# Kernel optimization log

Hardware: AMD Instinct MI355X
Metric: run time of the kernel (lower is better)

Reference implementation:

```python
import jax, jax.numpy as jnp
import numpy as np

C = 256          # channels
KS = 7           # kernel_size
G = 256          # groups (defaults to channels)
HID = C // 4     # hidden = channels // reduction
BN_EPS = 1e-5


def setup_inputs() -> dict:
    key = jax.random.key(0)
    ks = jax.random.split(key, 4)
    B, H, W = 4, 64, 64
    return {
        "x": jax.random.normal(ks[0], (B, C, H, W), jnp.float32),
        "reduce_w": jax.random.normal(ks[1], (HID, C), jnp.float32) / np.float32(np.sqrt(C)),
        "bn_gamma": jnp.ones((HID,), jnp.float32),
        "bn_beta": jnp.zeros((HID,), jnp.float32),
        "bn_mean": jnp.zeros((HID,), jnp.float32),
        "bn_var": jnp.ones((HID,), jnp.float32),
        "kproj_w": jax.random.normal(ks[2], (KS * KS * G, HID), jnp.float32) / np.float32(np.sqrt(HID)),
        "kproj_b": jnp.zeros((KS * KS * G,), jnp.float32),
    }


def _kernels(x, reduce_w, bn_gamma, bn_beta, bn_mean, bn_var, kproj_w, kproj_b):
    # 1x1 conv -> BN (eval mode) -> ReLU -> 1x1 conv, then per-pixel L2 kernel norm
    B, _, H, W = x.shape
    h = jnp.einsum('bchw,oc->bohw', x, reduce_w)
    inv = bn_gamma / jnp.sqrt(bn_var + BN_EPS)
    h = h * inv[None, :, None, None] + (bn_beta - bn_mean * inv)[None, :, None, None]
    h = jax.nn.relu(h)
    ker = jnp.einsum('bchw,oc->bohw', h, kproj_w) + kproj_b[None, :, None, None]
    ker = ker.reshape(B, G, KS * KS, H, W)           # (B, G, k*k, H, W)
    # kernel_norm == 'l2': zero-mean + unit L2 norm over the k*k taps
    ker = ker - ker.mean(axis=2, keepdims=True)
    denom = jnp.maximum(jnp.sqrt(jnp.sum(ker * ker, axis=2, keepdims=True)), 1e-6)
    return ker / denom


def reference(x, reduce_w, bn_gamma, bn_beta, bn_mean, bn_var, kproj_w, kproj_b):
    # get_kernels is under @torch.no_grad() in the original -> stop_gradient
    ker = jax.lax.stop_gradient(
        _kernels(x, reduce_w, bn_gamma, bn_beta, bn_mean, bn_var, kproj_w, kproj_b))
    B, Cc, H, W = x.shape
    pad = KS // 2
    gc = Cc // G  # = 1 for depthwise involution
    xp = jnp.pad(x, ((0, 0), (0, 0), (pad, pad), (pad, pad)))
    xg = xp.reshape(B, G, gc, H + 2 * pad, W + 2 * pad)
    # fused unfold-multiply-accumulate over the k*k taps (no (B,C,k,k,H,W) tensor)
    out = jnp.zeros((B, G, gc, H, W), x.dtype)
    for t in range(KS * KS):
        i, j = divmod(t, KS)
        out = out + xg[:, :, :, i:i + H, j:j + W] * ker[:, :, t][:, :, None]
    return out.reshape(B, Cc, H, W)
```

## Files before the change

### kernel.cpp

```cpp
#include <hip/hip_runtime.h>


#define C_    256
#define HID_  64
#define KS_   7
#define KK_   49
#define G_    256
#define H_    64
#define W_    64
#define HW_   4096
#define BN_EPS 1e-5f

typedef __attribute__((ext_vector_type(8)))  short bf16x8;
typedef __attribute__((ext_vector_type(4)))  float f32x4;
typedef __attribute__((ext_vector_type(16))) float f32x16;
typedef __attribute__((ext_vector_type(2)))  unsigned uv2;

__device__ __forceinline__ ushort f2bf(float f) {
    unsigned u = __float_as_uint(f);
    return (ushort)((u + 0x7fffu + ((u >> 16) & 1u)) >> 16);
}
__device__ __forceinline__ float bf2f(ushort s) {
    return __uint_as_float((unsigned)s << 16);
}
__device__ __forceinline__ float xor32p(float v) {
#if __has_builtin(__builtin_amdgcn_permlane32_swap)
    uv2 r = __builtin_amdgcn_permlane32_swap(__float_as_uint(v), __float_as_uint(v),
                                             false, false);
    return (__uint_as_float(r[0]) + __uint_as_float(r[1])) - v;
#else
    return __shfl_xor(v, 32);
#endif
}

__global__ __launch_bounds__(256) void prep_kernel(
    const float* __restrict__ kw, const float* __restrict__ kb,
    const float* __restrict__ reduce_w,
    const float* __restrict__ bn_gamma, const float* __restrict__ bn_beta,
    const float* __restrict__ bn_mean, const float* __restrict__ bn_var,
    ushort* __restrict__ kwb, float* __restrict__ rwT, float* __restrict__ betp,
    float* __restrict__ kbp)
{
    const int bid = blockIdx.x;
    if (bid < 256) {
        int idx  = bid * 256 + threadIdx.x;
        int base = idx * 16;
        int g    = base >> 12;
        int rem  = base & 4095;
        int t    = rem >> 6;
        int k0   = rem & 63;
        if (t >= 49 && ((t - 49) & 3) <= 1) return;
        union { ushort s[16]; uint4 v[2]; } u;
        if (t < KK_) {
            const float* src = kw + ((size_t)(g * KK_ + t)) * HID_ + k0;
            #pragma unroll
            for (int i = 0; i < 16; ++i) u.s[i] = f2bf(src[i]);
        } else {
            #pragma unroll
            for (int i = 0; i < 16; ++i) u.s[i] = 0;
        }
        uint4* dst = (uint4*)(kwb + base);
        dst[0] = u.v[0];
        dst[1] = u.v[1];
    } else if (bid == 256) {
        int k = threadIdx.x;
        #pragma unroll 1
        for (int o = 0; o < HID_; ++o) {
            float inv = bn_gamma[o] * rsqrtf(bn_var[o] + BN_EPS);
            rwT[k * HID_ + o] = reduce_w[o * C_ + k] * inv;
        }
        if (k < HID_) {
            float inv = bn_gamma[k] * rsqrtf(bn_var[k] + BN_EPS);
            betp[k] = bn_beta[k] - bn_mean[k] * inv;
        }
    } else if (bid == 257) {
        for (int i = threadIdx.x; i < G_ * 64; i += 256) {
            int g = i >> 6, t = i & 63;
            if (t >= 49 && ((t - 49) & 3) == 0) continue;
            kbp[i] = (t < KK_) ? kb[g * KK_ + t] : 0.f;
        }
    } else {
        const int g = bid - 258;
        __shared__ float part[4][64];
        const int k  = threadIdx.x & 63;
        const int pr = threadIdx.x >> 6;
        const int t0 = pr * 13;
        const int t1 = (t0 + 13 < KK_) ? t0 + 13 : KK_;
        float s = 0.f;
        for (int t = t0; t < t1; ++t)
            s += kw[((size_t)(g * KK_ + t)) * HID_ + k];
        part[pr][k] = s;
        __syncthreads();
        if (threadIdx.x < 64) {
            float u = part[0][k] + part[1][k] + part[2][k] + part[3][k];
            ushort uh = f2bf(u);
            ushort ul = f2bf(u - bf2f(uh));
            #pragma unroll
            for (int rr = 0; rr < 4; ++rr) {
                kwb[(size_t)g * 4096 + (49 + rr * 4) * 64 + k] = uh;
                kwb[(size_t)g * 4096 + (50 + rr * 4) * 64 + k] = ul;
            }
            float bs = (k < KK_) ? kb[g * KK_ + k] : 0.f;
            #pragma unroll
            for (int off = 32; off >= 1; off >>= 1) bs += __shfl_xor(bs, off);
            if (k == 0) {
                #pragma unroll
                for (int rr = 0; rr < 4; ++rr) kbp[g * 64 + 49 + rr * 4] = bs;
            }
        }
    }
}

__global__ __launch_bounds__(256) void hv1_kernel(
    const float* __restrict__ x, const float* __restrict__ rwT,
    float* __restrict__ hvp, int npx)
{
    const int lane = threadIdx.x & 63;
    const int wq   = __builtin_amdgcn_readfirstlane(threadIdx.x >> 6);
    const int kq   = blockIdx.y;
    const int p    = blockIdx.x * 64 + lane;
    const int b    = p >> 12;
    const int hw   = p & 4095;

    float acc[16];
    #pragma unroll
    for (int j = 0; j < 16; ++j) acc[j] = 0.f;

    const float* xp = x + ((size_t)b * C_ + kq * 64) * HW_ + hw;
    const float* rw = rwT + (kq * 64) * HID_ + wq * 16;
    #pragma unroll 8
    for (int kk = 0; kk < 64; ++kk) {
        float xk = xp[(size_t)kk * HW_];
        #pragma unroll
        for (int j = 0; j < 16; ++j) acc[j] = fmaf(xk, rw[kk * HID_ + j], acc[j]);
    }
    float* dst = hvp + ((size_t)(kq * 64 + wq * 16)) * npx + p;
    #pragma unroll
    for (int j = 0; j < 16; ++j) dst[(size_t)j * npx] = acc[j];
}

__global__ __launch_bounds__(256) void hv2_kernel(
    const float* __restrict__ hvp, const float* __restrict__ betp,
    ushort* __restrict__ hv, int npx)
{
    const int p  = blockIdx.x * 256 + threadIdx.x;
    const int o0 = blockIdx.y * 4;
    ushort s[4];
    #pragma unroll
    for (int j = 0; j < 4; ++j) {
        float v = 0.f;
        #pragma unroll
        for (int kq = 0; kq < 4; ++kq)
            v += hvp[(size_t)(kq * 64 + o0 + j) * npx + p];
        s[j] = f2bf(fmaxf(v + betp[o0 + j], 0.f));
    }
    uint2 w;
    w.x = (uint)s[0] | ((uint)s[1] << 16);
    w.y = (uint)s[2] | ((uint)s[3] << 16);
    *(uint2*)(hv + (size_t)p * HID_ + o0) = w;
}

__global__ __launch_bounds__(256) void invol_main(
    const float* __restrict__ x, const ushort* __restrict__ hv,
    const ushort* __restrict__ kwb, const float* __restrict__ kbp,
    float* __restrict__ out)
{
    __shared__ float x_s[38][72];
    __shared__ float hs_s[38][64];

    const int tid  = threadIdx.x;
    const int lane = tid & 63;
    const int wave = __builtin_amdgcn_readfirstlane(tid >> 6);
    const int bg   = blockIdx.x;
    const int b    = bg >> 8;
    const int g    = bg & 255;
    const int y0   = blockIdx.y << 5;
    const int l31  = lane & 31;
    const int h4   = (lane >> 5) * 4;
    const int kl16 = (lane >> 5) * 16;

    const float* xg = x + (size_t)bg * HW_;
    for (int idx = tid; idx < 38 * 72; idx += 256) {
        int r = idx / 72, c = idx - r * 72;
        int yy = y0 - 3 + r;
        int cc = c - 3;
        bool v = ((unsigned)yy < 64u) && ((unsigned)cc < 64u);
        x_s[r][c] = v ? xg[yy * 64 + cc] : 0.f;
    }

    bf16x8 ka[2][4];
    const char* kwg = (const char*)kwb + (size_t)g * 8192;
    #pragma unroll
    for (int m = 0; m < 2; ++m)
        #pragma unroll
        for (int s = 0; s < 4; ++s)
            ka[m][s] = *(const bf16x8*)(kwg + (m * 32 + l31) * 128 + s * 32 + kl16);
    f32x4 kv[2][4];
    #pragma unroll
    for (int m = 0; m < 2; ++m)
        #pragma unroll
        for (int q = 0; q < 4; ++q)
            kv[m][q] = *(const f32x4*)(kbp + g * 64 + m * 32 + q * 8 + h4);

    int po0[16], po1[9];
    #pragma unroll
    for (int r = 0; r < 16; ++r) {
        int T = (r & 3) + 8 * (r >> 2) + h4;
        int i = (T * 147) >> 10;
        int j = T - i * 7;
        po0[r] = i * 72 + j + l31;
    }
    #pragma unroll
    for (int r = 0; r < 9; ++r) {
        int T = 32 + (r & 3) + 8 * (r >> 2) + h4;
        int i = (T * 147) >> 10;
        int j = T - i * 7;
        po1[r] = i * 72 + j + l31;
    }

    __syncthreads();

    if (tid < 152) {
        int r  = tid >> 2;
        int c0 = (tid & 3) << 4;
        float v[22];
        #pragma unroll
        for (int i = 0; i < 22; ++i) v[i] = x_s[r][c0 + i];
        float s = v[0] + v[1] + v[2] + v[3] + v[4] + v[5] + v[6];
        hs_s[r][c0] = s;
        #pragma unroll
        for (int c = 1; c < 16; ++c) {
            s += v[c + 6] - v[c - 1];
            hs_s[r][c0 + c] = s;
        }
    }
    __syncthreads();

    const int rowpix0 = (b << 12) + (y0 << 6);

    #pragma unroll 2
    for (int rr = 0; rr < 8; ++rr) {
        const int ry = rr * 4 + wave;

        bf16x8 hb0[4], hb1[4];
        const char* hvrow = (const char*)hv + (size_t)(rowpix0 + (ry << 6)) * 128;
        #pragma unroll
        for (int s = 0; s < 4; ++s) {
            hb0[s] = *(const bf16x8*)(hvrow + l31 * 128 + s * 32 + kl16);
            hb1[s] = *(const bf16x8*)(hvrow + (32 + l31) * 128 + s * 32 + kl16);
        }

        float x2 = hs_s[ry][lane] + hs_s[ry + 1][lane] + hs_s[ry + 2][lane]
                 + hs_s[ry + 3][lane] + hs_s[ry + 4][lane]
                 + hs_s[ry + 5][lane] + hs_s[ry + 6][lane];

        f32x16 acc00, acc01, acc10, acc11;
        #pragma unroll
        for (int q = 0; q < 4; ++q)
            #pragma unroll
            for (int e = 0; e < 4; ++e) {
                acc00[q * 4 + e] = kv[0][q][e];
                acc01[q * 4 + e] = kv[0][q][e];
                acc10[q * 4 + e] = kv[1][q][e];
                acc11[q * 4 + e] = kv[1][q][e];
            }
        #pragma unroll
        for (int s = 0; s < 4; ++s) {
            acc00 = __builtin_amdgcn_mfma_f32_32x32x16_bf16(ka[0][s], hb0[s], acc00, 0, 0, 0);
            acc01 = __builtin_amdgcn_mfma_f32_32x32x16_bf16(ka[0][s], hb1[s], acc01, 0, 0, 0);
            acc10 = __builtin_amdgcn_mfma_f32_32x32x16_bf16(ka[1][s], hb0[s], acc10, 0, 0, 0);
            acc11 = __builtin_amdgcn_mfma_f32_32x32x16_bf16(ka[1][s], hb1[s], acc11, 0, 0, 0);
        }

        float ssq0 = 0.f, ssq1 = 0.f;
        #pragma unroll
        for (int r = 0; r < 16; ++r) {
            ssq0 = fmaf(acc00[r], acc00[r], ssq0);
            ssq1 = fmaf(acc01[r], acc01[r], ssq1);
        }
        #pragma unroll
        for (int r = 0; r < 9; ++r) {
            ssq0 = fmaf(acc10[r], acc10[r], ssq0);
            ssq1 = fmaf(acc11[r], acc11[r], ssq1);
        }
        float mn0 = (acc10[9] + acc10[10]) * (1.f / 49.f);
        float mn1 = (acc11[9] + acc11[10]) * (1.f / 49.f);

        float kx0 = 0.f, kx1 = 0.f;
        const float* xb = &x_s[0][0] + ry * 72;
        #pragma unroll
        for (int r = 0; r < 16; ++r) {
            float xv0 = xb[po0[r]];
            float xv1 = xb[po0[r] + 32];
            kx0 = fmaf(acc00[r], xv0, kx0);
            kx1 = fmaf(acc01[r], xv1, kx1);
        }
        #pragma unroll
        for (int r = 0; r < 9; ++r) {
            float xv0 = xb[po1[r]];
            float xv1 = xb[po1[r] + 32];
            kx0 = fmaf(acc10[r], xv0, kx0);
            kx1 = fmaf(acc11[r], xv1, kx1);
        }

        const bool lo = lane < 32;
        float kx_own = lo ? kx0 : kx1, kx_cr = lo ? kx1 : kx0;
        float ss_own = lo ? ssq0 : ssq1, ss_cr = lo ? ssq1 : ssq0;
        float mo     = lo ? mn0 : mn1;
        float kxo = kx_own + xor32p(kx_cr);
        float sso = ss_own + xor32p(ss_cr);

        float ss = fmaxf(sso - 49.f * mo * mo, 0.f);
        float is = 1.f / fmaxf(sqrtf(ss), 1e-6f);
        out[(size_t)bg * HW_ + ((y0 + ry) << 6) + lane] = (kxo - mo * x2) * is;
    }
}

__global__ __launch_bounds__(256) void hv_kernel(
    const float* __restrict__ x, const float* __restrict__ rwT,
    const float* __restrict__ betp, ushort* __restrict__ hv)
{
    const int lane = threadIdx.x & 63;
    const int q    = __builtin_amdgcn_readfirstlane(threadIdx.x >> 6);
    const int p    = blockIdx.x * 64 + lane;
    const int b    = p >> 12;
    const int hw   = p & 4095;
    float acc[16];
    #pragma unroll
    for (int j = 0; j < 16; ++j) acc[j] = betp[q * 16 + j];
    const float* xp = x + (size_t)b * C_ * HW_ + hw;
    #pragma unroll 8
    for (int k = 0; k < C_; ++k) {
        float xk = xp[(size_t)k * HW_];
        const float* rw = rwT + k * HID_ + q * 16;
        #pragma unroll
        for (int j = 0; j < 16; ++j) acc[j] = fmaf(xk, rw[j], acc[j]);
    }
    union { ushort s[16]; uint4 v[2]; } u;
    #pragma unroll
    for (int j = 0; j < 16; ++j) u.s[j] = f2bf(fmaxf(acc[j], 0.f));
    uint4* dst = (uint4*)(hv + (size_t)p * HID_ + q * 16);
    dst[0] = u.v[0];
    dst[1] = u.v[1];
}

__global__ __launch_bounds__(256) void invol_fallback(
    const float* __restrict__ x, const float* __restrict__ reduce_w,
    const float* __restrict__ bn_gamma, const float* __restrict__ bn_beta,
    const float* __restrict__ bn_mean, const float* __restrict__ bn_var,
    const float* __restrict__ kw, const float* __restrict__ kb,
    float* __restrict__ out)
{
    __shared__ float rwT[C_][HID_ + 4];
    __shared__ float bns[HID_];
    __shared__ float bnb[HID_];
    const int tid = threadIdx.x;
    const int b  = blockIdx.z;
    const int g0 = blockIdx.y * 32;
    const int p  = blockIdx.x * 256 + tid;
    const int py = p >> 6;
    const int px = p & 63;
    #pragma unroll 1
    for (int o = 0; o < HID_; ++o) rwT[tid][o] = reduce_w[o * C_ + tid];
    if (tid < HID_) {
        float inv = bn_gamma[tid] * rsqrtf(bn_var[tid] + BN_EPS);
        bns[tid] = inv;
        bnb[tid] = bn_beta[tid] - bn_mean[tid] * inv;
    }
    __syncthreads();
    float hvv[HID_];
    #pragma unroll
    for (int o = 0; o < HID_; ++o) hvv[o] = 0.f;
    const float* xb = x + (size_t)b * C_ * HW_ + p;
    #pragma unroll 4
    for (int k = 0; k < C_; ++k) {
        float xk = xb[(size_t)k * HW_];
        const float4* wr = (const float4*)&rwT[k][0];
        #pragma unroll
        for (int o4 = 0; o4 < HID_ / 4; ++o4) {
            float4 w = wr[o4];
            hvv[o4*4+0] = fmaf(xk, w.x, hvv[o4*4+0]);
            hvv[o4*4+1] = fmaf(xk, w.y, hvv[o4*4+1]);
            hvv[o4*4+2] = fmaf(xk, w.z, hvv[o4*4+2]);
            hvv[o4*4+3] = fmaf(xk, w.w, hvv[o4*4+3]);
        }
    }
    #pragma unroll
    for (int o = 0; o < HID_; ++o) hvv[o] = fmaxf(fmaf(hvv[o], bns[o], bnb[o]), 0.f);
    #pragma unroll 1
    for (int gi = 0; gi < 32; ++gi) {
        const int g = g0 + gi;
        const float* kwg = kw + (size_t)g * KK_ * HID_;
        float acc[KK_];
        #pragma unroll
        for (int t = 0; t < KK_; ++t) {
            float a = kb[g * KK_ + t];
            const float4* row = (const float4*)(kwg + t * HID_);
            #pragma unroll
            for (int k4 = 0; k4 < HID_ / 4; ++k4) {
                float4 w = row[k4];
                a = fmaf(w.x, hvv[k4*4+0], a);
                a = fmaf(w.y, hvv[k4*4+1], a);
                a = fmaf(w.z, hvv[k4*4+2], a);
                a = fmaf(w.w, hvv[k4*4+3], a);
            }
            acc[t] = a;
        }
        float mean = 0.f;
        #pragma unroll
        for (int t = 0; t < KK_; ++t) mean += acc[t];
        mean *= (1.f / 49.f);
        float ss = 0.f;
        #pragma unroll
        for (int t = 0; t < KK_; ++t) { acc[t] -= mean; ss = fmaf(acc[t], acc[t], ss); }
        float inv = 1.f / fmaxf(sqrtf(ss), 1e-6f);
        const float* xg = x + ((size_t)(b * G_ + g)) * HW_;
        float oacc = 0.f;
        #pragma unroll
        for (int i = 0; i < KS_; ++i) {
            int yv = py + i - 3;
            bool rok = ((unsigned)yv < (unsigned)H_);
            const float* xrow = xg + yv * W_;
            #pragma unroll
            for (int j = 0; j < KS_; ++j) {
                int xx = px + j - 3;
                bool ok = rok && ((unsigned)xx < (unsigned)W_);
                float v = ok ? xrow[xx] : 0.f;
                oacc = fmaf(v, acc[i*7+j], oacc);
            }
        }
        out[((size_t)(b * G_ + g)) * HW_ + p] = oacc * inv;
    }
}

extern "C" void kernel_launch(void* const* d_in, const int* in_sizes, int n_in,
                              void* d_out, int out_size, void* d_ws, size_t ws_size,
                              hipStream_t stream) {
    const float* x        = (const float*)d_in[0];
    const float* reduce_w = (const float*)d_in[1];
    const float* bn_gamma = (const float*)d_in[2];
    const float* bn_beta  = (const float*)d_in[3];
    const float* bn_mean  = (const float*)d_in[4];
    const float* bn_var   = (const float*)d_in[5];
    const float* kproj_w  = (const float*)d_in[6];
    const float* kproj_b  = (const float*)d_in[7];
    float* out = (float*)d_out;
    const int B   = in_sizes[0] / (C_ * HW_);
    const int npx = B * HW_;

    size_t kwb_off = 0;
    size_t kwb_sz  = (size_t)G_ * 64 * 64 * 2;
    size_t kbp_off = kwb_off + kwb_sz;
    size_t kbp_sz  = (size_t)G_ * 64 * 4;
    size_t rwt_off = kbp_off + kbp_sz;
    size_t rwt_sz  = (size_t)C_ * HID_ * 4;
    size_t bet_off = rwt_off + rwt_sz;
    size_t bet_sz  = 256;
    size_t hv_off  = bet_off + bet_sz;
    size_t hv_sz   = (size_t)npx * HID_ * 2;
    size_t hvp_off = hv_off + hv_sz;
    size_t hvp_sz  = (size_t)4 * HID_ * npx * 4;
    size_t need2   = hvp_off;
    size_t need    = hvp_off + hvp_sz;

    if (ws_size < need2) {
        dim3 grid(HW_ / 256, G_ / 32, B);
        invol_fallback<<<grid, 256, 0, stream>>>(x, reduce_w, bn_gamma, bn_beta,
                                                 bn_mean, bn_var, kproj_w, kproj_b, out);
        return;
    }

    ushort* kwb  = (ushort*)((char*)d_ws + kwb_off);
    float*  kbp  = (float*)((char*)d_ws + kbp_off);
    float*  rwT  = (float*)((char*)d_ws + rwt_off);
    float*  betp = (float*)((char*)d_ws + bet_off);
    ushort* hv   = (ushort*)((char*)d_ws + hv_off);
    float*  hvp  = (float*)((char*)d_ws + hvp_off);

    prep_kernel<<<dim3(258 + G_), 256, 0, stream>>>(kproj_w, kproj_b, reduce_w,
                                                    bn_gamma, bn_beta, bn_mean, bn_var,
                                                    kwb, rwT, betp, kbp);
    if (ws_size >= need) {
        hv1_kernel<<<dim3(npx / 64, 4), 256, 0, stream>>>(x, rwT, hvp, npx);
        hv2_kernel<<<dim3(npx / 256, 16), 256, 0, stream>>>(hvp, betp, hv, npx);
    } else {
        hv_kernel<<<dim3(npx / 64), 256, 0, stream>>>(x, rwT, betp, hv);
    }
    invol_main<<<dim3(B * G_, 2), 256, 0, stream>>>(x, hv, kwb, kbp, out);
}
```

Before: 130.9 us.

## Pad kernel taps to 7x8 layout and drop split-K hidden projection

Reorders the bf16 kernel-projection weights and biases so the 49 taps sit in a 7x8 padded grid (8 slots per kernel row). This lets the involution epilogue read shared-memory x values as contiguous 4-wide runs per tap row instead of using precomputed scattered offsets. It also loads the bias vectors inside the row loop rather than holding them in registers, which lowers register pressure. The two-stage split-K hidden projection (hv1/hv2 with an fp32 partial buffer) is removed in favour of the single-pass hv_kernel, saving one launch and the partial-sum traffic but giving up the extra parallelism of the split.

```diff
diff --git a/kernel.cpp b/kernel.cpp
--- a/kernel.cpp
+++ b/kernel.cpp
@@ -47,11 +47,12 @@
         int base = idx * 16;
         int g    = base >> 12;
         int rem  = base & 4095;
-        int t    = rem >> 6;
+        int tp   = rem >> 6;
         int k0   = rem & 63;
-        if (t >= 49 && ((t - 49) & 3) <= 1) return;
+        if (tp >= 56) return;
         union { ushort s[16]; uint4 v[2]; } u;
-        if (t < KK_) {
+        if ((tp & 7) < 7) {
+            int t = (tp >> 3) * 7 + (tp & 7);
             const float* src = kw + ((size_t)(g * KK_ + t)) * HID_ + k0;
             #pragma unroll
             for (int i = 0; i < 16; ++i) u.s[i] = f2bf(src[i]);
@@ -75,9 +76,9 @@
         }
     } else if (bid == 257) {
         for (int i = threadIdx.x; i < G_ * 64; i += 256) {
-            int g = i >> 6, t = i & 63;
-            if (t >= 49 && ((t - 49) & 3) == 0) continue;
-            kbp[i] = (t < KK_) ? kb[g * KK_ + t] : 0.f;
+            int g = i >> 6, tp = i & 63;
+            if (tp >= 56) continue;
+            kbp[i] = ((tp & 7) < 7) ? kb[g * KK_ + (tp >> 3) * 7 + (tp & 7)] : 0.f;
         }
     } else {
         const int g = bid - 258;
@@ -95,224 +96,21 @@
             float u = part[0][k] + part[1][k] + part[2][k] + part[3][k];
             ushort uh = f2bf(u);
             ushort ul = f2bf(u - bf2f(uh));
-            #pragma unroll
-            for (int rr = 0; rr < 4; ++rr) {
-                kwb[(size_t)g * 4096 + (49 + rr * 4) * 64 + k] = uh;
-                kwb[(size_t)g * 4096 + (50 + rr * 4) * 64 + k] = ul;
-            }
+            ushort* kg = kwb + (size_t)g * 4096;
+            kg[56 * 64 + k] = uh;  kg[60 * 64 + k] = uh;
+            kg[57 * 64 + k] = ul;  kg[61 * 64 + k] = ul;
+            kg[58 * 64 + k] = 0;   kg[59 * 64 + k] = 0;
+            kg[62 * 64 + k] = 0;   kg[63 * 64 + k] = 0;
             float bs = (k < KK_) ? kb[g * KK_ + k] : 0.f;
             #pragma unroll
             for (int off = 32; off >= 1; off >>= 1) bs += __shfl_xor(bs, off);
             if (k == 0) {
-                #pragma unroll
-                for (int rr = 0; rr < 4; ++rr) kbp[g * 64 + 49 + rr * 4] = bs;
-            }
-        }
-    }
-}
-
-__global__ __launch_bounds__(256) void hv1_kernel(
-    const float* __restrict__ x, const float* __restrict__ rwT,
-    float* __restrict__ hvp, int npx)
-{
-    const int lane = threadIdx.x & 63;
-    const int wq   = __builtin_amdgcn_readfirstlane(threadIdx.x >> 6);
-    const int kq   = blockIdx.y;
-    const int p    = blockIdx.x * 64 + lane;
-    const int b    = p >> 12;
-    const int hw   = p & 4095;
-
-    float acc[16];
-    #pragma unroll
-    for (int j = 0; j < 16; ++j) acc[j] = 0.f;
-
-    const float* xp = x + ((size_t)b * C_ + kq * 64) * HW_ + hw;
-    const float* rw = rwT + (kq * 64) * HID_ + wq * 16;
-    #pragma unroll 8
-    for (int kk = 0; kk < 64; ++kk) {
-        float xk = xp[(size_t)kk * HW_];
-        #pragma unroll
-        for (int j = 0; j < 16; ++j) acc[j] = fmaf(xk, rw[kk * HID_ + j], acc[j]);
-    }
-    float* dst = hvp + ((size_t)(kq * 64 + wq * 16)) * npx + p;
-    #pragma unroll
-    for (int j = 0; j < 16; ++j) dst[(size_t)j * npx] = acc[j];
-}
-
-__global__ __launch_bounds__(256) void hv2_kernel(
-    const float* __restrict__ hvp, const float* __restrict__ betp,
-    ushort* __restrict__ hv, int npx)
-{
-    const int p  = blockIdx.x * 256 + threadIdx.x;
-    const int o0 = blockIdx.y * 4;
-    ushort s[4];
-    #pragma unroll
-    for (int j = 0; j < 4; ++j) {
-        float v = 0.f;
-        #pragma unroll
-        for (int kq = 0; kq < 4; ++kq)
-            v += hvp[(size_t)(kq * 64 + o0 + j) * npx + p];
-        s[j] = f2bf(fmaxf(v + betp[o0 + j], 0.f));
-    }
-    uint2 w;
-    w.x = (uint)s[0] | ((uint)s[1] << 16);
-    w.y = (uint)s[2] | ((uint)s[3] << 16);
-    *(uint2*)(hv + (size_t)p * HID_ + o0) = w;
-}
-
-__global__ __launch_bounds__(256) void invol_main(
-    const float* __restrict__ x, const ushort* __restrict__ hv,
-    const ushort* __restrict__ kwb, const float* __restrict__ kbp,
-    float* __restrict__ out)
-{
-    __shared__ float x_s[38][72];
-    __shared__ float hs_s[38][64];
-
-    const int tid  = threadIdx.x;
-    const int lane = tid & 63;
-    const int wave = __builtin_amdgcn_readfirstlane(tid >> 6);
-    const int bg   = blockIdx.x;
-    const int b    = bg >> 8;
-    const int g    = bg & 255;
-    const int y0   = blockIdx.y << 5;
-    const int l31  = lane & 31;
-    const int h4   = (lane >> 5) * 4;
-    const int kl16 = (lane >> 5) * 16;
-
-    const float* xg = x + (size_t)bg * HW_;
-    for (int idx = tid; idx < 38 * 72; idx += 256) {
-        int r = idx / 72, c = idx - r * 72;
-        int yy = y0 - 3 + r;
-        int cc = c - 3;
-        bool v = ((unsigned)yy < 64u) && ((unsigned)cc < 64u);
-        x_s[r][c] = v ? xg[yy * 64 + cc] : 0.f;
-    }
-
-    bf16x8 ka[2][4];
-    const char* kwg = (const char*)kwb + (size_t)g * 8192;
-    #pragma unroll
-    for (int m = 0; m < 2; ++m)
-        #pragma unroll
-        for (int s = 0; s < 4; ++s)
-            ka[m][s] = *(const bf16x8*)(kwg + (m * 32 + l31) * 128 + s * 32 + kl16);
-    f32x4 kv[2][4];
-    #pragma unroll
-    for (int m = 0; m < 2; ++m)
-        #pragma unroll
-        for (int q = 0; q < 4; ++q)
-            kv[m][q] = *(const f32x4*)(kbp + g * 64 + m * 32 + q * 8 + h4);
-
-    int po0[16], po1[9];
-    #pragma unroll
-    for (int r = 0; r < 16; ++r) {
-        int T = (r & 3) + 8 * (r >> 2) + h4;
-        int i = (T * 147) >> 10;
-        int j = T - i * 7;
-        po0[r] = i * 72 + j + l31;
-    }
-    #pragma unroll
-    for (int r = 0; r < 9; ++r) {
-        int T = 32 + (r & 3) + 8 * (r >> 2) + h4;
-        int i = (T * 147) >> 10;
-        int j = T - i * 7;
-        po1[r] = i * 72 + j + l31;
-    }
-
-    __syncthreads();
-
-    if (tid < 152) {
-        int r  = tid >> 2;
-        int c0 = (tid & 3) << 4;
-        float v[22];
-        #pragma unroll
-        for (int i = 0; i < 22; ++i) v[i] = x_s[r][c0 + i];
-        float s = v[0] + v[1] + v[2] + v[3] + v[4] + v[5] + v[6];
-        hs_s[r][c0] = s;
-        #pragma unroll
-        for (int c = 1; c < 16; ++c) {
-            s += v[c + 6] - v[c - 1];
-            hs_s[r][c0 + c] = s;
-        }
-    }
-    __syncthreads();
-
-    const int rowpix0 = (b << 12) + (y0 << 6);
-
-    #pragma unroll 2
-    for (int rr = 0; rr < 8; ++rr) {
-        const int ry = rr * 4 + wave;
-
-        bf16x8 hb0[4], hb1[4];
-        const char* hvrow = (const char*)hv + (size_t)(rowpix0 + (ry << 6)) * 128;
-        #pragma unroll
-        for (int s = 0; s < 4; ++s) {
-            hb0[s] = *(const bf16x8*)(hvrow + l31 * 128 + s * 32 + kl16);
-            hb1[s] = *(const bf16x8*)(hvrow + (32 + l31) * 128 + s * 32 + kl16);
-        }
-
-        float x2 = hs_s[ry][lane] + hs_s[ry + 1][lane] + hs_s[ry + 2][lane]
-                 + hs_s[ry + 3][lane] + hs_s[ry + 4][lane]
-                 + hs_s[ry + 5][lane] + hs_s[ry + 6][lane];
-
-        f32x16 acc00, acc01, acc10, acc11;
-        #pragma unroll
-        for (int q = 0; q < 4; ++q)
-            #pragma unroll
-            for (int e = 0; e < 4; ++e) {
-                acc00[q * 4 + e] = kv[0][q][e];
-                acc01[q * 4 + e] = kv[0][q][e];
-                acc10[q * 4 + e] = kv[1][q][e];
-                acc11[q * 4 + e] = kv[1][q][e];
-            }
-        #pragma unroll
-        for (int s = 0; s < 4; ++s) {
-            acc00 = __builtin_amdgcn_mfma_f32_32x32x16_bf16(ka[0][s], hb0[s], acc00, 0, 0, 0);
-            acc01 = __builtin_amdgcn_mfma_f32_32x32x16_bf16(ka[0][s], hb1[s], acc01, 0, 0, 0);
-            acc10 = __builtin_amdgcn_mfma_f32_32x32x16_bf16(ka[1][s], hb0[s], acc10, 0, 0, 0);
-            acc11 = __builtin_amdgcn_mfma_f32_32x32x16_bf16(ka[1][s], hb1[s], acc11, 0, 0, 0);
-        }
-
-        float ssq0 = 0.f, ssq1 = 0.f;
-        #pragma unroll
-        for (int r = 0; r < 16; ++r) {
-            ssq0 = fmaf(acc00[r], acc00[r], ssq0);
-            ssq1 = fmaf(acc01[r], acc01[r], ssq1);
-        }
-        #pragma unroll
-        for (int r = 0; r < 9; ++r) {
-            ssq0 = fmaf(acc10[r], acc10[r], ssq0);
-            ssq1 = fmaf(acc11[r], acc11[r], ssq1);
-        }
-        float mn0 = (acc10[9] + acc10[10]) * (1.f / 49.f);
-        float mn1 = (acc11[9] + acc11[10]) * (1.f / 49.f);
-
-        float kx0 = 0.f, kx1 = 0.f;
-        const float* xb = &x_s[0][0] + ry * 72;
-        #pragma unroll
-        for (int r = 0; r < 16; ++r) {
-            float xv0 = xb[po0[r]];
-            float xv1 = xb[po0[r] + 32];
-            kx0 = fmaf(acc00[r], xv0, kx0);
-            kx1 = fmaf(acc01[r], xv1, kx1);
-        }
-        #pragma unroll
-        for (int r = 0; r < 9; ++r) {
-            float xv0 = xb[po1[r]];
-            float xv1 = xb[po1[r] + 32];
-            kx0 = fmaf(acc10[r], xv0, kx0);
-            kx1 = fmaf(acc11[r], xv1, kx1);
-        }
-
-        const bool lo = lane < 32;
-        float kx_own = lo ? kx0 : kx1, kx_cr = lo ? kx1 : kx0;
-        float ss_own = lo ? ssq0 : ssq1, ss_cr = lo ? ssq1 : ssq0;
-        float mo     = lo ? mn0 : mn1;
-        float kxo = kx_own + xor32p(kx_cr);
-        float sso = ss_own + xor32p(ss_cr);
-
-        float ss = fmaxf(sso - 49.f * mo * mo, 0.f);
-        float is = 1.f / fmaxf(sqrtf(ss), 1e-6f);
-        out[(size_t)bg * HW_ + ((y0 + ry) << 6) + lane] = (kxo - mo * x2) * is;
+                float* bg = kbp + g * 64;
+                bg[56] = bs; bg[60] = bs;
+                bg[57] = 0.f; bg[58] = 0.f; bg[59] = 0.f;
+                bg[61] = 0.f; bg[62] = 0.f; bg[63] = 0.f;
+            }
+        }
     }
 }
 
@@ -342,6 +140,152 @@
     uint4* dst = (uint4*)(hv + (size_t)p * HID_ + q * 16);
     dst[0] = u.v[0];
     dst[1] = u.v[1];
+}
+
+__global__ __launch_bounds__(256) void invol_main(
+    const float* __restrict__ x, const ushort* __restrict__ hv,
+    const ushort* __restrict__ kwb, const float* __restrict__ kbp,
+    float* __restrict__ out)
+{
+    __shared__ float x_s[38][72];
+    __shared__ float hs_s[38][64];
+
+    const int tid  = threadIdx.x;
+    const int lane = tid & 63;
+    const int wave = __builtin_amdgcn_readfirstlane(tid >> 6);
+    const int bg   = blockIdx.x;
+    const int b    = bg >> 8;
+    const int g    = bg & 255;
+    const int y0   = blockIdx.y << 5;
+    const int l31  = lane & 31;
+    const int h4   = (lane >> 5) * 4;
+    const int kl16 = (lane >> 5) * 16;
+    const int c0   = h4 + l31;
+
+    const float* xg = x + (size_t)bg * HW_;
+    for (int idx = tid; idx < 38 * 72; idx += 256) {
+        int r = idx / 72, c = idx - r * 72;
+        int yy = y0 - 3 + r;
+        int cc = c - 3;
+        bool v = ((unsigned)yy < 64u) && ((unsigned)cc < 64u);
+        x_s[r][c] = v ? xg[yy * 64 + cc] : 0.f;
+    }
+
+    bf16x8 ka[2][4];
+    const char* kwg = (const char*)kwb + (size_t)g * 8192;
+    #pragma unroll
+    for (int m = 0; m < 2; ++m)
+        #pragma unroll
+        for (int s = 0; s < 4; ++s)
+            ka[m][s] = *(const bf16x8*)(kwg + (m * 32 + l31) * 128 + s * 32 + kl16);
+    const float* kbg = kbp + g * 64 + h4;
+
+    __syncthreads();
+
+    if (tid < 152) {
+        int r  = tid >> 2;
+        int cc0 = (tid & 3) << 4;
+        float v[22];
+        #pragma unroll
+        for (int i = 0; i < 22; ++i) v[i] = x_s[r][cc0 + i];
+        float s = v[0] + v[1] + v[2] + v[3] + v[4] + v[5] + v[6];
+        hs_s[r][cc0] = s;
+        #pragma unroll
+        for (int c = 1; c < 16; ++c) {
+            s += v[c + 6] - v[c - 1];
+            hs_s[r][cc0 + c] = s;
+        }
+    }
+    __syncthreads();
+
+    const int rowpix0 = (b << 12) + (y0 << 6);
+
+    #pragma unroll 2
+    for (int rr = 0; rr < 8; ++rr) {
+        const int ry = rr * 4 + wave;
+
+        bf16x8 hb0[4], hb1[4];
+        const char* hvrow = (const char*)hv + (size_t)(rowpix0 + (ry << 6)) * 128;
+        #pragma unroll
+        for (int s = 0; s < 4; ++s) {
+            hb0[s] = *(const bf16x8*)(hvrow + l31 * 128 + s * 32 + kl16);
+            hb1[s] = *(const bf16x8*)(hvrow + (32 + l31) * 128 + s * 32 + kl16);
+        }
+        f32x4 kv0[4], kv1[4];
+        #pragma unroll
+        for (int q = 0; q < 4; ++q) {
+            kv0[q] = *(const f32x4*)(kbg + q * 8);
+            kv1[q] = *(const f32x4*)(kbg + 32 + q * 8);
+        }
+
+        float x2 = hs_s[ry][lane] + hs_s[ry + 1][lane] + hs_s[ry + 2][lane]
+                 + hs_s[ry + 3][lane] + hs_s[ry + 4][lane]
+                 + hs_s[ry + 5][lane] + hs_s[ry + 6][lane];
+
+        f32x16 acc00, acc01, acc10, acc11;
+        #pragma unroll
+        for (int q = 0; q < 4; ++q)
+            #pragma unroll
+            for (int e = 0; e < 4; ++e) {
+                acc00[q * 4 + e] = kv0[q][e];
+                acc01[q * 4 + e] = kv0[q][e];
+                acc10[q * 4 + e] = kv1[q][e];
+                acc11[q * 4 + e] = kv1[q][e];
+            }
+        #pragma unroll
+        for (int s = 0; s < 4; ++s) {
+            acc00 = __builtin_amdgcn_mfma_f32_32x32x16_bf16(ka[0][s], hb0[s], acc00, 0, 0, 0);
+            acc01 = __builtin_amdgcn_mfma_f32_32x32x16_bf16(ka[0][s], hb1[s], acc01, 0, 0, 0);
+            acc10 = __builtin_amdgcn_mfma_f32_32x32x16_bf16(ka[1][s], hb0[s], acc10, 0, 0, 0);
+            acc11 = __builtin_amdgcn_mfma_f32_32x32x16_bf16(ka[1][s], hb1[s], acc11, 0, 0, 0);
+        }
+
+        float ssq0 = 0.f, ssq1 = 0.f;
+        #pragma unroll
+        for (int r = 0; r < 16; ++r) {
+            ssq0 = fmaf(acc00[r], acc00[r], ssq0);
+            ssq1 = fmaf(acc01[r], acc01[r], ssq1);
+        }
+        #pragma unroll
+        for (int r = 0; r < 12; ++r) {
+            ssq0 = fmaf(acc10[r], acc10[r], ssq0);
+            ssq1 = fmaf(acc11[r], acc11[r], ssq1);
+        }
+        float mn0 = (acc10[12] + acc10[13]) * (1.f / 49.f);
+        float mn1 = (acc11[12] + acc11[13]) * (1.f / 49.f);
+
+        float kx0 = 0.f, kx1 = 0.f;
+        const float* xb = &x_s[ry][0];
+        #pragma unroll
+        for (int q = 0; q < 4; ++q) {
+            const float* bp = xb + q * 72 + c0;
+            #pragma unroll
+            for (int e = 0; e < 4; ++e) {
+                kx0 = fmaf(acc00[q * 4 + e], bp[e], kx0);
+                kx1 = fmaf(acc01[q * 4 + e], bp[32 + e], kx1);
+            }
+        }
+        #pragma unroll
+        for (int q = 0; q < 3; ++q) {
+            const float* bp = xb + (4 + q) * 72 + c0;
+            #pragma unroll
+            for (int e = 0; e < 4; ++e) {
+                kx0 = fmaf(acc10[q * 4 + e], bp[e], kx0);
+                kx1 = fmaf(acc11[q * 4 + e], bp[32 + e], kx1);
+            }
+        }
+
+        const bool lo = lane < 32;
+        float kx_own = lo ? kx0 : kx1, kx_cr = lo ? kx1 : kx0;
+        float ss_own = lo ? ssq0 : ssq1, ss_cr = lo ? ssq1 : ssq0;
+        float mo     = lo ? mn0 : mn1;
+        float kxo = kx_own + xor32p(kx_cr);
+        float sso = ss_own + xor32p(ss_cr);
+
+        float ss = fmaxf(sso - 49.f * mo * mo, 0.f);
+        float is = 1.f / fmaxf(sqrtf(ss), 1e-6f);
+        out[(size_t)bg * HW_ + ((y0 + ry) << 6) + lane] = (kxo - mo * x2) * is;
+    }
 }
 
 __global__ __launch_bounds__(256) void invol_fallback(
@@ -458,12 +402,9 @@
     size_t bet_sz  = 256;
     size_t hv_off  = bet_off + bet_sz;
     size_t hv_sz   = (size_t)npx * HID_ * 2;
-    size_t hvp_off = hv_off + hv_sz;
-    size_t hvp_sz  = (size_t)4 * HID_ * npx * 4;
-    size_t need2   = hvp_off;
-    size_t need    = hvp_off + hvp_sz;
-
-    if (ws_size < need2) {
+    size_t need    = hv_off + hv_sz;
+
+    if (ws_size < need) {
         dim3 grid(HW_ / 256, G_ / 32, B);
         invol_fallback<<<grid, 256, 0, stream>>>(x, reduce_w, bn_gamma, bn_beta,
                                                  bn_mean, bn_var, kproj_w, kproj_b, out);
@@ -475,16 +416,10 @@
     float*  rwT  = (float*)((char*)d_ws + rwt_off);
     float*  betp = (float*)((char*)d_ws + bet_off);
     ushort* hv   = (ushort*)((char*)d_ws + hv_off);
-    float*  hvp  = (float*)((char*)d_ws + hvp_off);
 
     prep_kernel<<<dim3(258 + G_), 256, 0, stream>>>(kproj_w, kproj_b, reduce_w,
                                                     bn_gamma, bn_beta, bn_mean, bn_var,
                                                     kwb, rwT, betp, kbp);
-    if (ws_size >= need) {
-        hv1_kernel<<<dim3(npx / 64, 4), 256, 0, stream>>>(x, rwT, hvp, npx);
-        hv2_kernel<<<dim3(npx / 256, 16), 256, 0, stream>>>(hvp, betp, hv, npx);
-    } else {
-        hv_kernel<<<dim3(npx / 64), 256, 0, stream>>>(x, rwT, betp, hv);
-    }
+    hv_kernel<<<dim3(npx / 64), 256, 0, stream>>>(x, rwT, betp, hv);
     invol_main<<<dim3(B * G_, 2), 256, 0, stream>>>(x, hv, kwb, kbp, out);
 }
```

After: 140.8 us. +7.6%, slower.
